# Kernel tuning notes

Measured on AMD Instinct MI355X. Metric: run time of the kernel, lower is better.

## Reference

```python
import jax, jax.numpy as jnp
import numpy as np

VOCAB, HIDDEN, LAYERS = 128, 1024, 2
B, T = 128, 512


def setup_inputs() -> dict:
    key = jax.random.key(0)
    ks = jax.random.split(key, 8)
    s0 = 1.0 / np.sqrt(HIDDEN)
    x = jax.random.normal(ks[0], (B, T, VOCAB), dtype=jnp.float32)
    h = jnp.zeros((LAYERS, B, HIDDEN), dtype=jnp.float32)
    c = jnp.zeros((LAYERS, B, HIDDEN), dtype=jnp.float32)
    # LSTM params, gate order (i, f, g, o) concatenated along last dim (4H)
    Wx0 = jax.random.uniform(ks[1], (VOCAB, 4 * HIDDEN), jnp.float32, -s0, s0)
    Wh0 = jax.random.uniform(ks[2], (HIDDEN, 4 * HIDDEN), jnp.float32, -s0, s0)
    b0 = jax.random.uniform(ks[3], (4 * HIDDEN,), jnp.float32, -s0, s0)
    Wx1 = jax.random.uniform(ks[4], (HIDDEN, 4 * HIDDEN), jnp.float32, -s0, s0)
    Wh1 = jax.random.uniform(ks[5], (HIDDEN, 4 * HIDDEN), jnp.float32, -s0, s0)
    b1 = jax.random.uniform(ks[6], (4 * HIDDEN,), jnp.float32, -s0, s0)
    return {"x": x, "h": h, "c": c, "Wx0": Wx0, "Wh0": Wh0, "b0": b0,
            "Wx1": Wx1, "Wh1": Wh1, "b1": b1}


def _lstm_cell(inp, h_prev, c_prev, Wx, Wh, b):
    gates = inp @ Wx + h_prev @ Wh + b            # (B, 4H)
    i, f, g, o = jnp.split(gates, 4, axis=-1)
    i = jax.nn.sigmoid(i)
    f = jax.nn.sigmoid(f)
    g = jnp.tanh(g)
    o = jax.nn.sigmoid(o)
    c_new = f * c_prev + i * g
    h_new = o * jnp.tanh(c_new)
    return h_new, c_new


def reference(x, h, c, Wx0, Wh0, b0, Wx1, Wh1, b1):
    layer_params = [(Wx0, Wh0, b0), (Wx1, Wh1, b1)]

    def step(carry, x_t):
        h_prev, c_prev = carry                    # each (L, B, H)
        inp = x_t                                 # (B, VOCAB)
        hs, cs = [], []
        for l, (Wx, Wh, b) in enumerate(layer_params):
            h_new, c_new = _lstm_cell(inp, h_prev[l], c_prev[l], Wx, Wh, b)
            hs.append(h_new)
            cs.append(c_new)
            inp = h_new
        return (jnp.stack(hs), jnp.stack(cs)), hs[-1]

    xs = jnp.swapaxes(x, 0, 1)                    # (T, B, VOCAB)
    (h_f, c_f), outs = jax.lax.scan(step, (h, c), xs)
    outs = jnp.swapaxes(outs, 0, 1)               # (B, T, H)
    return outs, h_f, c_f
```

## Files before the change

kernel.cpp:

```cpp
#include <hip/hip_runtime.h>

#define VV 128
#define HH 1024
#define BB 128
#define TT 512
#define G4 4096
#define BTH ((size_t)BB * TT * HH)
#define HPAR (4 * 64 * 512)
#define RING 256

typedef __attribute__((ext_vector_type(8))) short bf16x8;
typedef __attribute__((ext_vector_type(16))) float f32x16;

__device__ __forceinline__ short f2bf(float f) {
  unsigned u = __float_as_uint(f);
  u = (u + 0x7fffu + ((u >> 16) & 1u)) >> 16;
  return (short)u;
}

__device__ __forceinline__ float fsig(float x) {
  x = fminf(fmaxf(x, -30.f), 30.f);
  float e = __expf(-x);
  return 1.f / (1.f + e);
}
__device__ __forceinline__ float ftanh(float x) {
  x = fminf(fmaxf(x, -15.f), 15.f);
  float e = __expf(-2.f * x);
  return (1.f - e) / (1.f + e);
}

__device__ __forceinline__ unsigned eidx(int t) {
  return ((unsigned)(t + 1) * 37u) & (RING - 1);
}


__global__ void conv_x(const float* __restrict__ x, short* __restrict__ xp) {
  const int n = TT * 4 * 8 * 512;
  for (int i = blockIdx.x * blockDim.x + threadIdx.x; i < n; i += gridDim.x * blockDim.x) {
    int e = i & 7, lane = (i >> 3) & 63, kc = (i >> 9) & 7, rb = (i >> 12) & 3, t = i >> 14;
    int row = rb * 32 + (lane & 31);
    int v = kc * 16 + ((lane >> 5) << 3) + e;
    xp[i] = f2bf(x[((size_t)row * TT + t) * VV + v]);
  }
}

__global__ void init_state(const float* __restrict__ h,
                           short* __restrict__ h0dst, short* __restrict__ h1dst) {
  const int n = 2 * HPAR;
  for (int i = blockIdx.x * blockDim.x + threadIdx.x; i < n; i += gridDim.x * blockDim.x) {
    int inner = i & (HPAR - 1);
    int l = i >> 17;
    int e = i & 7, lane = (i >> 3) & 63, kc = (i >> 9) & 63, rb = (i >> 15) & 3;
    int row = rb * 32 + (lane & 31);
    int j = kc * 16 + ((lane >> 5) << 3) + e;
    short hb = f2bf(h[((size_t)l * BB + row) * HH + j]);
    (l ? h1dst : h0dst)[inner] = hb;
  }
}

__global__ void pack_w(const float* __restrict__ Wx0, const float* __restrict__ Wh0,
                       const float* __restrict__ Wx1, const float* __restrict__ Wh1,
                       short* __restrict__ wp0, short* __restrict__ wp1) {
  const int n0 = 128 * 72 * 512;
  const int n1 = 128 * 128 * 512;
  for (int i = blockIdx.x * blockDim.x + threadIdx.x; i < n0 + n1; i += gridDim.x * blockDim.x) {
    if (i < n0) {
      int cu = i / (72 * 512);
      int rem = i - cu * (72 * 512);
      int kc = rem >> 9, le = rem & 511;
      int lane = le >> 3, e = le & 7;
      int k = kc * 16 + ((lane >> 5) << 3) + e;
      int cl = lane & 31;
      int gcol = (cl >> 3) * HH + cu * 8 + (cl & 7);
      float f = (k < VV) ? Wx0[(size_t)k * G4 + gcol] : Wh0[(size_t)(k - VV) * G4 + gcol];
      wp0[i] = f2bf(f);
    } else {
      int j = i - n0;
      int cu = j >> 16;
      int rem = j & 65535;
      int kc = rem >> 9, le = rem & 511;
      int lane = le >> 3, e = le & 7;
      int k = kc * 16 + ((lane >> 5) << 3) + e;
      int cl = lane & 31;
      int gcol = (cl >> 3) * HH + cu * 8 + (cl & 7);
      float f = (k < HH) ? Wx1[(size_t)k * G4 + gcol] : Wh1[(size_t)(k - HH) * G4 + gcol];
      wp1[j] = f2bf(f);
    }
  }
}

__global__ void pack_b(const float* __restrict__ b0, const float* __restrict__ b1,
                       float* __restrict__ bp, unsigned* __restrict__ slots) {
  int i = blockIdx.x * blockDim.x + threadIdx.x;
  if (i < 2 * 128 * 32) {
    int l = i >> 12;
    int cu = (i >> 5) & 127;
    int cc = i & 31;
    const float* b = l ? b1 : b0;
    bp[i] = b[(cc >> 3) * HH + cu * 8 + (cc & 7)];
  }
  if (i < 512) slots[i] = 0u;
}


template <int NCH, bool COH>
__device__ __forceinline__ void hgemm(f32x16* acc, const short* pa0, const short* pa1,
                                      const short* __restrict__ pb) {
  constexpr int NG = NCH / 16;
  bf16x8 A[3][16];
#pragma unroll
  for (int g = 0; g < 3; ++g) {
#pragma unroll
    for (int j = 0; j < 16; ++j) {
      const int c = g * 16 + j;
      const short* ap = (c < 64) ? (pa0 + c * 512) : (pa1 + (c - 64) * 512);
      if constexpr (COH)
        asm volatile("global_load_dwordx4 %0, %1, off sc0 sc1" : "=v"(A[g][j]) : "v"(ap));
      else
        asm volatile("global_load_dwordx4 %0, %1, off sc0" : "=v"(A[g][j]) : "v"(ap));
    }
  }
#pragma unroll
  for (int g = 0; g < NG; ++g) {
    const int rem = NG - 1 - g;
    if (rem >= 2)      asm volatile("s_waitcnt vmcnt(32)" ::: "memory");
    else if (rem == 1) asm volatile("s_waitcnt vmcnt(16)" ::: "memory");
    else               asm volatile("s_waitcnt vmcnt(0)" ::: "memory");
#pragma unroll
    for (int j = 0; j < 16; ++j)
      asm volatile("" : "+v"(A[g % 3][j]));
#pragma unroll
    for (int j = 0; j < 16; ++j) {
      const int c = g * 16 + j;
      bf16x8 b = *(const bf16x8*)(pb + c * 512);
      acc[j & 3] = __builtin_amdgcn_mfma_f32_32x32x16_bf16(A[g % 3][j], b, acc[j & 3], 0, 0, 0);
    }
    if (g + 3 < NG) {
#pragma unroll
      for (int j = 0; j < 16; ++j) {
        const int c = (g + 3) * 16 + j;
        const short* ap = (c < 64) ? (pa0 + c * 512) : (pa1 + (c - 64) * 512);
        if constexpr (COH)
          asm volatile("global_load_dwordx4 %0, %1, off sc0 sc1"
                       : "=v"(A[(g + 3) % 3][j]) : "v"(ap));
        else
          asm volatile("global_load_dwordx4 %0, %1, off sc0"
                       : "=v"(A[(g + 3) % 3][j]) : "v"(ap));
      }
    }
  }
}

__device__ __forceinline__ void xgemm(f32x16* acc, const short* __restrict__ pax,
                                      const short* __restrict__ pb) {
#pragma unroll
  for (int c = 0; c < 8; ++c) {
    bf16x8 a = *(const bf16x8*)(pax + c * 512);
    bf16x8 b = *(const bf16x8*)(pb + c * 512);
    acc[c & 3] = __builtin_amdgcn_mfma_f32_32x32x16_bf16(a, b, acc[c & 3], 0, 0, 0);
  }
}

template <bool RINGM>
__global__ void __launch_bounds__(256, 1) lstm_main(const short* __restrict__ xp,
    short* __restrict__ h0b, short* __restrict__ h1b,
    const short* __restrict__ wp0, const short* __restrict__ wp1,
    const float* __restrict__ bpack, const float* __restrict__ cin,
    float* __restrict__ out, unsigned* __restrict__ slots) {
  __shared__ short wlds[128 * 512];
  unsigned* gdone = slots + 256;
  const int blk = blockIdx.x;
  const int layer = blk >> 7;
  const int cu = blk & 127;
  const int tid = threadIdx.x;
  const int lane = tid & 63;
  const int wave = tid >> 6;

  const int nkc = layer ? 128 : 72;
  const short* wsrc = layer ? (wp1 + (size_t)cu * 128 * 512) : (wp0 + (size_t)cu * 72 * 512);
  for (int i = tid; i < nkc * 64; i += 256)
    ((int4*)wlds)[i] = ((const int4*)wsrc)[i];
  __syncthreads();

  const int col = lane & 31;
  const float bias = bpack[layer * 4096 + cu * 32 + col];
  const int uu = col & 7;
  const bool ewlane = (col < 8);
  const int gcol = cu * 8 + uu;
  const int hi4 = ((lane >> 5) << 2);

  float creg[16], hval[16];
#pragma unroll
  for (int r = 0; r < 16; ++r) {
    int grow = wave * 32 + (r & 3) + ((r >> 2) << 3) + hi4;
    creg[r] = ewlane ? cin[(size_t)layer * BB * HH + (size_t)grow * HH + gcol] : 0.f;
    hval[r] = 0.f;
  }

  const int pst = (wave * 64 + (cu >> 1)) * 512 + ((cu & 1) << 8);
  const int wv64 = wave * 64 * 512 + lane * 8;

  f32x16 acc[4];
  auto initacc = [&]() {
#pragma unroll
    for (int r = 0; r < 16; ++r) {
      acc[0][r] = bias; acc[1][r] = 0.f; acc[2][r] = 0.f; acc[3][r] = 0.f;
    }
  };

  if (layer == 0) {
    initacc();
    xgemm(acc, xp + ((size_t)(0 * 4 + wave) * 8) * 512 + lane * 8, wlds + lane * 8);
  }

  for (int p = 0; p <= TT; ++p) {
    if (p > 0) {
      const unsigned tgt = (unsigned)p;
      if ((blk & 31) == 0 && tid < 32) {
        for (;;) {
          unsigned v = __hip_atomic_load(&slots[blk + tid],
                                         __ATOMIC_RELAXED, __HIP_MEMORY_SCOPE_AGENT);
          if (__all(v >= tgt)) break;
          __builtin_amdgcn_s_sleep(1);
        }
        if (tid == 0)
          __hip_atomic_store(&gdone[(blk >> 5) << 5], tgt,
                             __ATOMIC_RELAXED, __HIP_MEMORY_SCOPE_AGENT);
      }
      if (tid < 8) {
        for (;;) {
          unsigned v = __hip_atomic_load(&gdone[tid << 5],
                                         __ATOMIC_RELAXED, __HIP_MEMORY_SCOPE_AGENT);
          if (__all(v >= tgt)) break;
          __builtin_amdgcn_s_sleep(1);
        }
      }
      __syncthreads();
    }

    const bool active = layer ? (p >= 1) : (p < TT);
    const int t = layer ? (p - 1) : p;
    if (active) {
      const short *ra0, *ra1;
      if constexpr (RINGM) {
        ra0 = h0b + (size_t)eidx(p - 1) * HPAR + wv64;
        ra1 = h1b + (size_t)eidx(p - 2) * HPAR + wv64;
      } else {
        const int parR = (p + 1) & 1;
        ra0 = h0b + (size_t)parR * HPAR + wv64;
        ra1 = h1b + (size_t)(p & 1) * HPAR + wv64;
      }
      if (layer == 0) {
        hgemm<64, !RINGM>(acc, ra0, ra0, wlds + 8 * 512 + lane * 8);
      } else {
        initacc();
        hgemm<128, !RINGM>(acc, ra0, ra1, wlds + lane * 8);
      }
      f32x16 accf = (acc[0] + acc[1]) + (acc[2] + acc[3]);
      short* hp;
      if constexpr (RINGM)
        hp = layer ? (h1b + (size_t)eidx(p - 1) * HPAR)
                   : (h0b + (size_t)eidx(p) * HPAR);
      else
        hp = layer ? (h1b + (size_t)((p + 1) & 1) * HPAR)
                   : (h0b + (size_t)(p & 1) * HPAR);
#pragma unroll
      for (int r = 0; r < 16; ++r) {
        float a0 = accf[r];
        float nl = (col >= 16 && col < 24) ? ftanh(a0) : fsig(a0);
        float f_ = __shfl_xor(nl, 8);
        float g_ = __shfl_xor(nl, 16);
        float o_ = __shfl_xor(nl, 24);
        const int rloc = (r & 3) + ((r >> 2) << 3) + hi4;
        const int grow = wave * 32 + rloc;
        float hnew = 0.f;
        if (ewlane) {
          float cnew = f_ * creg[r] + nl * g_;
          creg[r] = cnew;
          hnew = o_ * ftanh(cnew);
          hval[r] = hnew;
        }
        unsigned hb = (unsigned short)f2bf(hnew);
        unsigned pb2 = (unsigned)__shfl_xor((int)hb, 1);
        if (ewlane) {
          if (t == TT - 1) {
            out[BTH + (size_t)layer * BB * HH + (size_t)grow * HH + gcol] = hnew;
            out[BTH + (size_t)(2 + layer) * BB * HH + (size_t)grow * HH + gcol] = creg[r];
          }
          if (!(uu & 1)) {
            unsigned dw = hb | (pb2 << 16);
            __hip_atomic_store((unsigned*)(hp + pst + rloc * 8 + uu), dw,
                               __ATOMIC_RELAXED, __HIP_MEMORY_SCOPE_AGENT);
          }
        }
      }
    }

    if (p == TT) {
      if (layer && active && ewlane) {
#pragma unroll
        for (int r = 0; r < 16; ++r) {
          const int rloc = (r & 3) + ((r >> 2) << 3) + hi4;
          const int grow = wave * 32 + rloc;
          out[(size_t)grow * TT * HH + (size_t)t * HH + gcol] = hval[r];
        }
      }
      break;
    }

    __syncthreads();
    if (tid == 0)
      __hip_atomic_store(&slots[blk], (unsigned)(p + 1),
                         __ATOMIC_RELAXED, __HIP_MEMORY_SCOPE_AGENT);

    if (layer == 0) {
      if (p + 1 < TT) {
        initacc();
        xgemm(acc, xp + ((size_t)((p + 1) * 4 + wave) * 8) * 512 + lane * 8, wlds + lane * 8);
      }
    } else if (active && ewlane) {
#pragma unroll
      for (int r = 0; r < 16; ++r) {
        const int rloc = (r & 3) + ((r >> 2) << 3) + hi4;
        const int grow = wave * 32 + rloc;
        out[(size_t)grow * TT * HH + (size_t)t * HH + gcol] = hval[r];
      }
    }
  }
}


extern "C" void kernel_launch(void* const* d_in, const int* in_sizes, int n_in,
                              void* d_out, int out_size, void* d_ws, size_t ws_size,
                              hipStream_t stream) {
  const float* x   = (const float*)d_in[0];
  const float* h   = (const float*)d_in[1];
  const float* c   = (const float*)d_in[2];
  const float* Wx0 = (const float*)d_in[3];
  const float* Wh0 = (const float*)d_in[4];
  const float* b0  = (const float*)d_in[5];
  const float* Wx1 = (const float*)d_in[6];
  const float* Wh1 = (const float*)d_in[7];
  const float* b1  = (const float*)d_in[8];
  float* out = (float*)d_out;

  char* ws = (char*)d_ws;
  short* xp  = (short*)ws;
  short* wp0 = (short*)(ws + 16777216);
  short* wp1 = (short*)(ws + 26214400);
  float* bp  = (float*)(ws + 42991616);
  unsigned* slots = (unsigned*)(ws + 43024384);
  short* h0p = (short*)(ws + 43026432);
  short* h1p = (short*)(ws + 43550720);
  short* h0r = (short*)(ws + 44075008);
  short* h1r = (short*)(ws + 111183872);
  const size_t need_ring = 178292736;

  const bool ring = (ws_size >= need_ring);
  short* h0 = ring ? h0r : h0p;
  short* h1 = ring ? h1r : h1p;
  short* h0ini = ring ? h0r : (h0p + HPAR);
  short* h1ini = ring ? h1r : (h1p + HPAR);

  hipLaunchKernelGGL(conv_x,     dim3(2048), dim3(256), 0, stream, x, xp);
  hipLaunchKernelGGL(init_state, dim3(512),  dim3(256), 0, stream, h, h0ini, h1ini);
  hipLaunchKernelGGL(pack_w,     dim3(4096), dim3(256), 0, stream, Wx0, Wh0, Wx1, Wh1, wp0, wp1);
  hipLaunchKernelGGL(pack_b,     dim3(32),   dim3(256), 0, stream, b0, b1, bp, slots);

  if (ring)
    hipLaunchKernelGGL((lstm_main<true>), dim3(256), dim3(256), 0, stream,
                       xp, h0, h1, wp0, wp1, bp, c, out, slots);
  else
    hipLaunchKernelGGL((lstm_main<false>), dim3(256), dim3(256), 0, stream,
                       xp, h0, h1, wp0, wp1, bp, c, out, slots);
}
```

Before: 6.379 ms.

## Fuse input bf16 conversion into main LSTM kernel and shrink h ring

Drops the separate conv_x pre-pass that repacked x to bf16 and instead has each layer-0 lane load raw fp32 x rows and convert them to bf16 in registers just before the input MFMA. The ring of hidden-state buffers shrinks from 256 to 32 slots, and the workspace layout is compacted to match. This removes one kernel launch and a full read/write pass over x, plus a smaller ring footprint that may be more cache friendly. The cost is extra conversion ALU work and uncoalesced fp32 loads on the layer-0 critical path each step, and a shorter ring reuses slots sooner.

```diff
diff --git a/kernel.cpp b/kernel.cpp
--- a/kernel.cpp
+++ b/kernel.cpp
@@ -7,7 +7,7 @@
 #define G4 4096
 #define BTH ((size_t)BB * TT * HH)
 #define HPAR (4 * 64 * 512)
-#define RING 256
+#define RING 32
 
 typedef __attribute__((ext_vector_type(8))) short bf16x8;
 typedef __attribute__((ext_vector_type(16))) float f32x16;
@@ -33,16 +33,6 @@
   return ((unsigned)(t + 1) * 37u) & (RING - 1);
 }
 
-
-__global__ void conv_x(const float* __restrict__ x, short* __restrict__ xp) {
-  const int n = TT * 4 * 8 * 512;
-  for (int i = blockIdx.x * blockDim.x + threadIdx.x; i < n; i += gridDim.x * blockDim.x) {
-    int e = i & 7, lane = (i >> 3) & 63, kc = (i >> 9) & 7, rb = (i >> 12) & 3, t = i >> 14;
-    int row = rb * 32 + (lane & 31);
-    int v = kc * 16 + ((lane >> 5) << 3) + e;
-    xp[i] = f2bf(x[((size_t)row * TT + t) * VV + v]);
-  }
-}
 
 __global__ void init_state(const float* __restrict__ h,
                            short* __restrict__ h0dst, short* __restrict__ h1dst) {
@@ -151,18 +141,22 @@
   }
 }
 
-__device__ __forceinline__ void xgemm(f32x16* acc, const short* __restrict__ pax,
-                                      const short* __restrict__ pb) {
+__device__ __forceinline__ void xgemm_raw(f32x16* acc, const float* __restrict__ xlane,
+                                          const short* __restrict__ pb) {
 #pragma unroll
   for (int c = 0; c < 8; ++c) {
-    bf16x8 a = *(const bf16x8*)(pax + c * 512);
+    float4 lo = *(const float4*)(xlane + c * 16);
+    float4 hi = *(const float4*)(xlane + c * 16 + 4);
+    bf16x8 a;
+    a[0] = f2bf(lo.x); a[1] = f2bf(lo.y); a[2] = f2bf(lo.z); a[3] = f2bf(lo.w);
+    a[4] = f2bf(hi.x); a[5] = f2bf(hi.y); a[6] = f2bf(hi.z); a[7] = f2bf(hi.w);
     bf16x8 b = *(const bf16x8*)(pb + c * 512);
     acc[c & 3] = __builtin_amdgcn_mfma_f32_32x32x16_bf16(a, b, acc[c & 3], 0, 0, 0);
   }
 }
 
 template <bool RINGM>
-__global__ void __launch_bounds__(256, 1) lstm_main(const short* __restrict__ xp,
+__global__ void __launch_bounds__(256, 1) lstm_main(const float* __restrict__ x,
     short* __restrict__ h0b, short* __restrict__ h1b,
     const short* __restrict__ wp0, const short* __restrict__ wp1,
     const float* __restrict__ bpack, const float* __restrict__ cin,
@@ -188,6 +182,9 @@
   const bool ewlane = (col < 8);
   const int gcol = cu * 8 + uu;
   const int hi4 = ((lane >> 5) << 2);
+  const int arow = wave * 32 + col;
+  const int koff = (lane >> 5) << 3;
+  const float* xlane0 = x + (size_t)arow * (TT * VV) + koff;
 
   float creg[16], hval[16];
 #pragma unroll
@@ -210,7 +207,7 @@
 
   if (layer == 0) {
     initacc();
-    xgemm(acc, xp + ((size_t)(0 * 4 + wave) * 8) * 512 + lane * 8, wlds + lane * 8);
+    xgemm_raw(acc, xlane0, wlds + lane * 8);
   }
 
   for (int p = 0; p <= TT; ++p) {
@@ -246,8 +243,7 @@
         ra0 = h0b + (size_t)eidx(p - 1) * HPAR + wv64;
         ra1 = h1b + (size_t)eidx(p - 2) * HPAR + wv64;
       } else {
-        const int parR = (p + 1) & 1;
-        ra0 = h0b + (size_t)parR * HPAR + wv64;
+        ra0 = h0b + (size_t)((p + 1) & 1) * HPAR + wv64;
         ra1 = h1b + (size_t)(p & 1) * HPAR + wv64;
       }
       if (layer == 0) {
@@ -316,7 +312,7 @@
     if (layer == 0) {
       if (p + 1 < TT) {
         initacc();
-        xgemm(acc, xp + ((size_t)((p + 1) * 4 + wave) * 8) * 512 + lane * 8, wlds + lane * 8);
+        xgemm_raw(acc, xlane0 + (size_t)(p + 1) * VV, wlds + lane * 8);
       }
     } else if (active && ewlane) {
 #pragma unroll
@@ -345,32 +341,28 @@
   float* out = (float*)d_out;
 
   char* ws = (char*)d_ws;
-  short* xp  = (short*)ws;
-  short* wp0 = (short*)(ws + 16777216);
-  short* wp1 = (short*)(ws + 26214400);
-  float* bp  = (float*)(ws + 42991616);
-  unsigned* slots = (unsigned*)(ws + 43024384);
-  short* h0p = (short*)(ws + 43026432);
-  short* h1p = (short*)(ws + 43550720);
-  short* h0r = (short*)(ws + 44075008);
-  short* h1r = (short*)(ws + 111183872);
-  const size_t need_ring = 178292736;
+  short* wp0 = (short*)ws;
+  short* wp1 = (short*)(ws + 9437184);
+  float* bp  = (float*)(ws + 26214400);
+  unsigned* slots = (unsigned*)(ws + 26247168);
+  short* h0r = (short*)(ws + 26249216);
+  short* h1r = (short*)(ws + 34637824);
+  const size_t need_ring = 43026432;
+  short* h0p = h0r;
+  short* h1p = (short*)(ws + 26249216 + 1048576);
 
   const bool ring = (ws_size >= need_ring);
-  short* h0 = ring ? h0r : h0p;
-  short* h1 = ring ? h1r : h1p;
   short* h0ini = ring ? h0r : (h0p + HPAR);
   short* h1ini = ring ? h1r : (h1p + HPAR);
 
-  hipLaunchKernelGGL(conv_x,     dim3(2048), dim3(256), 0, stream, x, xp);
   hipLaunchKernelGGL(init_state, dim3(512),  dim3(256), 0, stream, h, h0ini, h1ini);
   hipLaunchKernelGGL(pack_w,     dim3(4096), dim3(256), 0, stream, Wx0, Wh0, Wx1, Wh1, wp0, wp1);
   hipLaunchKernelGGL(pack_b,     dim3(32),   dim3(256), 0, stream, b0, b1, bp, slots);
 
   if (ring)
     hipLaunchKernelGGL((lstm_main<true>), dim3(256), dim3(256), 0, stream,
-                       xp, h0, h1, wp0, wp1, bp, c, out, slots);
+                       x, h0r, h1r, wp0, wp1, bp, c, out, slots);
   else
     hipLaunchKernelGGL((lstm_main<false>), dim3(256), dim3(256), 0, stream,
-                       xp, h0, h1, wp0, wp1, bp, c, out, slots);
-}
+                       x, h0p, h1p, wp0, wp1, bp, c, out, slots);
+}
```

After: 6.489 ms. About the same (+1.7%).
